# Kernel tuning notes

Measured on AMD Instinct MI355X. Metric: run time of the kernel, lower is better.

## Reference

```python
import jax, jax.numpy as jnp
import numpy as np

NH = 8      # num_head
WIN = 7     # window
EPS = 1e-6


def _ln(x, w, b):
    m = x.mean(-1, keepdims=True)
    v = ((x - m) ** 2).mean(-1, keepdims=True)
    return (x - m) / jnp.sqrt(v + EPS) * w + b


def _dwconv(x, w, b):
    # x: [B,H,W,Cc], w: [7,7,1,Cc] (HWIO), depthwise (groups=Cc)
    y = jax.lax.conv_general_dilated(
        x, w, window_strides=(1, 1), padding='SAME',
        dimension_numbers=('NHWC', 'HWIO', 'NHWC'),
        feature_group_count=x.shape[-1])
    return y + b


def setup_inputs() -> dict:
    B, H, W, C = 16, 56, 56, 256
    RATIO = 8
    key = jax.random.key(0)
    ki = iter(jax.random.split(key, 48))
    def lin(i, o):
        return jax.random.normal(next(ki), (i, o), jnp.float32) * (1.0 / i) ** 0.5
    def bias(o):
        return jnp.zeros((o,), jnp.float32)
    def dw(c):
        return jax.random.normal(next(ki), (7, 7, 1, c), jnp.float32) * 0.05
    inp = {
        'x':   jax.random.normal(next(ki), (B, H, W, C), jnp.float32),
        'x_e': jax.random.normal(next(ki), (B, H, W, C // 2), jnp.float32),
        # LayerNorms
        'norm_w': jnp.ones((C,), jnp.float32),  'norm_b': bias(C),
        'norme_w': jnp.ones((C // 2,), jnp.float32), 'norme_b': bias(C // 2),
        # local_rr path
        'rr1_w': lin(C, C), 'rr1_b': bias(C),
        'rr2_w': lin(C, C), 'rr2_b': bias(C),
        'rr3_w': lin(C, C), 'rr3_b': bias(C),
        'conv_w': dw(C), 'conv_b': bias(C),
        # LocalAttentionRGBT
        'lx_l1_w': lin(C, C // 2), 'lx_l1_b': bias(C // 2),
        'lx_l2_w': lin(C // 2, C // 2), 'lx_l2_b': bias(C // 2),
        'lx_c1_w': dw(C // 2), 'lx_c1_b': bias(C // 2),
        'lx_c2_w': dw(C // 2), 'lx_c2_b': bias(C // 2),
        'lx_fc1_w': lin(C, C // RATIO),  # no bias
        'lx_fc2_w': lin(C // RATIO, C),  # no bias
        'lx_l3_w': lin(C, C // 2), 'lx_l3_b': bias(C // 2),
        # global pooled attention
        'kv_w': lin(C, C), 'kv_b': bias(C),
        'q_w': lin(C // 2 * 3, C // 2), 'q_b': bias(C // 2),
        # output projections (window != 0 => in = 2C)
        'proj_w': lin(2 * C, C), 'proj_b': bias(C),
        'proje_w': lin(2 * C, C // 2), 'proje_b': bias(C // 2),
    }
    return inp


def reference(x, x_e, norm_w, norm_b, norme_w, norme_b,
              rr1_w, rr1_b, rr2_w, rr2_b, rr3_w, rr3_b, conv_w, conv_b,
              lx_l1_w, lx_l1_b, lx_l2_w, lx_l2_b, lx_c1_w, lx_c1_b,
              lx_c2_w, lx_c2_b, lx_fc1_w, lx_fc2_w, lx_l3_w, lx_l3_b,
              kv_w, kv_b, q_w, q_b, proj_w, proj_b, proje_w, proje_b):
    B, H, W, C = x.shape
    hd = C // NH // 2  # head dim
    x = _ln(x, norm_w, norm_b)
    x_e = _ln(x_e, norme_w, norme_b)

    # --- local_rr: gated depthwise-conv branch ---
    rr1 = x @ rr1_w + rr1_b
    rr2 = _dwconv(x @ rr2_w + rr2_b, conv_w, conv_b)
    rr2 = rr2 @ rr3_w + rr3_b
    local_rr = rr1 * rr2  # [B,H,W,C]

    # --- LocalAttentionRGBT: cross-modal cosine-sim channel gate ---
    rgb = x @ lx_l1_w + lx_l1_b      # [B,H,W,C/2]
    t = x_e @ lx_l2_w + lx_l2_b      # [B,H,W,C/2]
    co = _dwconv(rgb * t, lx_c1_w, lx_c1_b)
    di = _dwconv(jnp.abs(rgb - t), lx_c2_w, lx_c2_b)
    co_di = jnp.concatenate([co, di], axis=-1)           # [B,H,W,C]
    amap = co_di.mean(-1, keepdims=True)                 # [B,H,W,1]
    dot = (amap * co_di).sum((1, 2), keepdims=True)      # [B,1,1,C]
    n1 = jnp.sqrt((amap ** 2).sum((1, 2), keepdims=True))
    n2 = jnp.sqrt((co_di ** 2).sum((1, 2), keepdims=True))
    cos_sim = dot / (n1 * n2 + 1e-6)                     # [B,1,1,C]
    attn_c = jax.nn.sigmoid(
        jax.nn.gelu(cos_sim @ lx_fc1_w, approximate=False) @ lx_fc2_w)
    local_rx = (co_di * attn_c) @ lx_l3_w + lx_l3_b      # [B,H,W,C/2]

    # --- global: pooled-q full-kv attention ---
    kv = (x @ kv_w + kv_b).reshape(B, H * W, 2, NH, hd).transpose(2, 0, 3, 1, 4)
    k, v = kv[0], kv[1]                                  # [B,NH,HW,hd]
    rx = jnp.concatenate([x, x_e], axis=-1)              # [B,H,W,3C/2]
    rx_pool = rx.reshape(B, WIN, H // WIN, WIN, W // WIN, -1).mean((2, 4))  # [B,7,7,3C/2]
    q = (rx_pool @ q_w + q_b).reshape(B, WIN * WIN, NH, hd).transpose(0, 2, 1, 3)
    scores = jnp.einsum('bnqd,bnkd->bnqk', q * hd ** -0.5, k)  # [B,NH,49,HW]
    attn = jax.nn.softmax(scores, axis=-1)
    g = jnp.einsum('bnqk,bnkd->bnqd', attn, v)           # [B,NH,49,hd]
    g = g.reshape(B, NH, WIN, WIN, hd).transpose(0, 1, 4, 2, 3).reshape(B, C // 2, WIN, WIN)
    g = jax.image.resize(g, (B, C // 2, H, W), method='bilinear')  # align_corners=False
    g = g.transpose(0, 2, 3, 1)                          # [B,H,W,C/2]

    cat = jnp.concatenate([local_rr, local_rx, g], axis=-1)  # [B,H,W,2C]
    x_e_out = cat @ proje_w + proje_b
    x_out = cat @ proj_w + proj_b
    return (x_out, x_e_out)
```

## Files before the change

### kernel.cpp

```cpp
#include <hip/hip_runtime.h>
#include <hip/hip_bf16.h>
#include <cstdint>
#include <cstddef>

#define N_TOK 50176
#define HWSZ  3136
#define BATCH 16

#define GF_MUL     1
#define GF_ASCALE  2
#define GF_KVSPLIT 4
#define GF_DUAL    8

typedef __hip_bfloat16 bf16;
typedef __attribute__((ext_vector_type(8))) short bf16x8;
typedef __attribute__((ext_vector_type(4))) float f32x4;
typedef __attribute__((ext_vector_type(4))) unsigned short u16x4;

__device__ __forceinline__ void  stf(float* p, size_t i, float v) { p[i] = v; }
__device__ __forceinline__ void  stf(bf16* p, size_t i, float v) { p[i] = __float2bfloat16(v); }
__device__ __forceinline__ float bu2f(unsigned short u) {
    unsigned int x = ((unsigned int)u) << 16; float f; __builtin_memcpy(&f, &x, 4); return f;
}
__device__ __forceinline__ unsigned short f2bu(float f) {
    bf16 t = __float2bfloat16(f); unsigned short u; __builtin_memcpy(&u, &t, 2); return u;
}

struct WtrDesc { const float* src; bf16* dst; int K; int N; int off; };
struct WtrPack { WtrDesc d[9]; int total; };
__global__ __launch_bounds__(256) void wtr_all(WtrPack p)
{
    int idx = blockIdx.x * 256 + threadIdx.x;
    if (idx >= p.total) return;
    #pragma unroll
    for (int s = 0; s < 9; s++) {
        int lo = p.d[s].off, hi = lo + p.d[s].K * p.d[s].N;
        if (idx >= lo && idx < hi) {
            int j = idx - lo;
            int k = j / p.d[s].N, n = j % p.d[s].N;
            p.d[s].dst[(size_t)n * p.d[s].K + k] = __float2bfloat16(p.d[s].src[j]);
        }
    }
}

__global__ __launch_bounds__(256) void ln_kernel(const float* __restrict__ in,
    const float* __restrict__ w, const float* __restrict__ b,
    bf16* __restrict__ out, int rows, int Cdim)
{
    int wave = threadIdx.x >> 6, lane = threadIdx.x & 63;
    int row = blockIdx.x * 4 + wave;
    if (row >= rows) return;
    const float* p = in + (size_t)row * Cdim;
    int nj = Cdim >> 6;
    float v[4];
    float s = 0.f;
    for (int j = 0; j < nj; j++) { v[j] = p[lane + 64 * j]; s += v[j]; }
    for (int off = 32; off; off >>= 1) s += __shfl_xor(s, off, 64);
    float mean = s / (float)Cdim;
    float vs = 0.f;
    for (int j = 0; j < nj; j++) { float d = v[j] - mean; vs += d * d; }
    for (int off = 32; off; off >>= 1) vs += __shfl_xor(vs, off, 64);
    float rstd = 1.f / sqrtf(vs / (float)Cdim + 1e-6f);
    bf16* q = out + (size_t)row * Cdim;
    for (int j = 0; j < nj; j++) {
        int c = lane + 64 * j;
        q[c] = __float2bfloat16((v[j] - mean) * rstd * w[c] + b[c]);
    }
}

#define LDT 56
template<int FLAGS, typename OT>
__global__ __launch_bounds__(256) void gemm_mfma(
    const bf16* __restrict__ A, int lda,
    const bf16* __restrict__ WT,
    const float* __restrict__ bias,
    OT* __restrict__ C, int ldc,
    int M, int K, int N,
    const bf16* __restrict__ mul, int mulld,
    const float* __restrict__ ascale,
    bf16* __restrict__ kout, bf16* __restrict__ vout,
    OT* __restrict__ C2, int ldc2, const float* __restrict__ bias2, int N1)
{
    __shared__ bf16 As[64][LDT];
    __shared__ bf16 Bs[128][LDT];
    int ntile = N >> 7;
    int bid = blockIdx.x;
    bid = (bid & 7) * (gridDim.x >> 3) + (bid >> 3);
    int m0 = (bid / ntile) * 64;
    int n0 = (bid % ntile) * 128;
    int tid = threadIdx.x;
    int lane = tid & 63, wid = tid >> 6;
    int wc = wid * 32;
    int lrow = lane & 15, lko = (lane >> 4) * 8;
    int sr = tid >> 2, sko = (tid & 3) * 8;

    f32x4 acc[4][2];
    #pragma unroll
    for (int i = 0; i < 4; i++)
        #pragma unroll
        for (int j = 0; j < 2; j++)
            acc[i][j] = (f32x4){0.f, 0.f, 0.f, 0.f};

    bf16x8 ra, rb[2];
    {
        bf16x8 v = *reinterpret_cast<const bf16x8*>(A + (size_t)(m0 + sr) * lda + sko);
        if (FLAGS & GF_ASCALE) {
            int bidx = (m0 + sr) / HWSZ;
            const float* as = ascale + (size_t)bidx * K + sko;
            #pragma unroll
            for (int e = 0; e < 8; e++)
                v[e] = (short)f2bu(bu2f((unsigned short)v[e]) * as[e]);
        }
        ra = v;
        rb[0] = *reinterpret_cast<const bf16x8*>(WT + (size_t)(n0 + sr) * K + sko);
        rb[1] = *reinterpret_cast<const bf16x8*>(WT + (size_t)(n0 + sr + 64) * K + sko);
    }

    for (int k0 = 0; k0 < K; k0 += 32) {
        *reinterpret_cast<bf16x8*>(&As[sr][sko]) = ra;
        *reinterpret_cast<bf16x8*>(&Bs[sr][sko]) = rb[0];
        *reinterpret_cast<bf16x8*>(&Bs[sr + 64][sko]) = rb[1];
        __syncthreads();
        int kn = k0 + 32;
        if (kn < K) {
            bf16x8 v = *reinterpret_cast<const bf16x8*>(A + (size_t)(m0 + sr) * lda + kn + sko);
            if (FLAGS & GF_ASCALE) {
                int bidx = (m0 + sr) / HWSZ;
                const float* as = ascale + (size_t)bidx * K + kn + sko;
                #pragma unroll
                for (int e = 0; e < 8; e++)
                    v[e] = (short)f2bu(bu2f((unsigned short)v[e]) * as[e]);
            }
            ra = v;
            rb[0] = *reinterpret_cast<const bf16x8*>(WT + (size_t)(n0 + sr) * K + kn + sko);
            rb[1] = *reinterpret_cast<const bf16x8*>(WT + (size_t)(n0 + sr + 64) * K + kn + sko);
        }
        bf16x8 af[4], br[2];
        #pragma unroll
        for (int i = 0; i < 4; i++)
            af[i] = *reinterpret_cast<const bf16x8*>(&As[i * 16 + lrow][lko]);
        #pragma unroll
        for (int j = 0; j < 2; j++)
            br[j] = *reinterpret_cast<const bf16x8*>(&Bs[wc + j * 16 + lrow][lko]);
        #pragma unroll
        for (int i = 0; i < 4; i++)
            #pragma unroll
            for (int j = 0; j < 2; j++)
                acc[i][j] = __builtin_amdgcn_mfma_f32_16x16x32_bf16(af[i], br[j], acc[i][j], 0, 0, 0);
        __syncthreads();
    }

    int orow = (lane >> 4) * 4;
    int ocol = lane & 15;
    #pragma unroll
    for (int i = 0; i < 4; i++) {
        #pragma unroll
        for (int j = 0; j < 2; j++) {
            #pragma unroll
            for (int p = 0; p < 4; p++) {
                int gm = m0 + i * 16 + orow + p;
                int gn = n0 + wc + j * 16 + ocol;
                if (FLAGS & GF_KVSPLIT) {
                    float v = acc[i][j][p] + bias[gn];
                    int bb = gm / HWSZ, n = gm % HWSZ;
                    if (gn < 128)
                        kout[(((size_t)bb * 8 + (gn >> 4)) * HWSZ + n) * 16 + (gn & 15)] = __float2bfloat16(v);
                    else {
                        int hh = (gn - 128) >> 4, dd = (gn - 128) & 15;
                        vout[(((size_t)bb * 8 + hh) * 16 + dd) * HWSZ + n] = __float2bfloat16(v);
                    }
                } else if (FLAGS & GF_DUAL) {
                    if (gn < N1) {
                        float v = acc[i][j][p] + bias[gn];
                        stf(C, (size_t)gm * ldc + gn, v);
                    } else {
                        float v = acc[i][j][p] + bias2[gn - N1];
                        stf(C2, (size_t)gm * ldc2 + (gn - N1), v);
                    }
                } else {
                    float v = acc[i][j][p] + bias[gn];
                    if (FLAGS & GF_MUL) v *= __bfloat162float(mul[(size_t)gm * mulld + gn]);
                    stf(C, (size_t)gm * ldc + gn, v);
                }
            }
        }
    }
}

__global__ __launch_bounds__(256) void gemm_k(
    const float* __restrict__ A, int lda,
    const float* __restrict__ Wt, const float* __restrict__ bias,
    float* __restrict__ Cc, int ldc, int M, int K, int Nc)
{
    __shared__ float As[16][68];
    __shared__ float Ws[16][64];
    int ntile = Nc >> 6;
    int tile_n = blockIdx.x % ntile;
    int tile_m = blockIdx.x / ntile;
    int m0 = tile_m * 64, n0 = tile_n * 64;
    int tid = threadIdx.x;
    int tx = tid & 15, ty = tid >> 4;
    float acc[4][4] = {};
    for (int k0 = 0; k0 < K; k0 += 16) {
        int ks = tid & 15, ms = tid >> 4;
        #pragma unroll
        for (int i = 0; i < 4; i++) {
            int gm = m0 + ms + i * 16;
            As[ks][ms + i * 16] = (gm < M) ? A[(size_t)gm * lda + k0 + ks] : 0.f;
        }
        #pragma unroll
        for (int j = 0; j < 4; j++) {
            int k = (tid >> 6) * 4 + j;
            Ws[k][tid & 63] = Wt[(size_t)(k0 + k) * Nc + n0 + (tid & 63)];
        }
        __syncthreads();
        #pragma unroll
        for (int k = 0; k < 16; k++) {
            float a[4], w[4];
            #pragma unroll
            for (int i = 0; i < 4; i++) a[i] = As[k][ty * 4 + i];
            #pragma unroll
            for (int j = 0; j < 4; j++) w[j] = Ws[k][tx * 4 + j];
            #pragma unroll
            for (int i = 0; i < 4; i++)
                #pragma unroll
                for (int j = 0; j < 4; j++)
                    acc[i][j] += a[i] * w[j];
        }
        __syncthreads();
    }
    #pragma unroll
    for (int i = 0; i < 4; i++) {
        int gm = m0 + ty * 4 + i;
        if (gm >= M) continue;
        #pragma unroll
        for (int j = 0; j < 4; j++) {
            int gn = n0 + tx * 4 + j;
            Cc[(size_t)gm * ldc + gn] = acc[i][j] + bias[gn];
        }
    }
}

__global__ __launch_bounds__(256) void dwconv_reg(const bf16* __restrict__ in,
    bf16* __restrict__ out,
    const float* __restrict__ w0, const float* __restrict__ b0,
    const float* __restrict__ w1, const float* __restrict__ b1, int split)
{
    int tid = threadIdx.x;
    int chg = tid & 31;
    int bsw = (blockIdx.x & 7) * 196 + (blockIdx.x >> 3);
    int pg  = bsw * 8 + (tid >> 5);
    int xg = pg % 14;
    int y  = (pg / 14) % 56;
    int b  = pg / (14 * 56);
    int c0 = chg * 8;
    int x0 = xg * 4;

    const float* wp; const float* bp; int ws, cw;
    if (c0 < split) { wp = w0; bp = b0; ws = split;       cw = c0; }
    else            { wp = w1; bp = b1; ws = 256 - split; cw = c0 - split; }

    float acc[4][8];
    #pragma unroll
    for (int o = 0; o < 4; o++)
        #pragma unroll
        for (int e = 0; e < 8; e++) acc[o][e] = 0.f;

    const bf16* base = in + (size_t)b * HWSZ * 256 + c0;
    const float* wbase = wp + cw;
    #pragma unroll
    for (int ky = 0; ky < 7; ky++) {
        int gy = y + ky - 3;
        if (gy < 0 || gy >= 56) continue;
        const bf16* rowp = base + (size_t)gy * 56 * 256;
        float cf[10][8];
        #pragma unroll
        for (int j = 0; j < 10; j++) {
            int gx = x0 + j - 3;
            bf16x8 v = {0, 0, 0, 0, 0, 0, 0, 0};
            if ((unsigned)gx < 56u)
                v = *reinterpret_cast<const bf16x8*>(rowp + (size_t)gx * 256);
            #pragma unroll
            for (int e = 0; e < 8; e++) cf[j][e] = bu2f((unsigned short)v[e]);
        }
        const float* wrow = wbase + ky * 7 * ws;
        #pragma unroll
        for (int kx = 0; kx < 7; kx++) {
            float4 wa = *reinterpret_cast<const float4*>(wrow + kx * ws);
            float4 wb = *reinterpret_cast<const float4*>(wrow + kx * ws + 4);
            #pragma unroll
            for (int o = 0; o < 4; o++) {
                acc[o][0] += cf[o + kx][0] * wa.x;
                acc[o][1] += cf[o + kx][1] * wa.y;
                acc[o][2] += cf[o + kx][2] * wa.z;
                acc[o][3] += cf[o + kx][3] * wa.w;
                acc[o][4] += cf[o + kx][4] * wb.x;
                acc[o][5] += cf[o + kx][5] * wb.y;
                acc[o][6] += cf[o + kx][6] * wb.z;
                acc[o][7] += cf[o + kx][7] * wb.w;
            }
        }
    }

    float4 ba = *reinterpret_cast<const float4*>(bp + cw);
    float4 bb = *reinterpret_cast<const float4*>(bp + cw + 4);
    bf16* obase = out + (((size_t)b * HWSZ + (size_t)y * 56 + x0) * 256) + c0;
    #pragma unroll
    for (int o = 0; o < 4; o++) {
        bf16x8 ov;
        ov[0] = (short)f2bu(acc[o][0] + ba.x);
        ov[1] = (short)f2bu(acc[o][1] + ba.y);
        ov[2] = (short)f2bu(acc[o][2] + ba.z);
        ov[3] = (short)f2bu(acc[o][3] + ba.w);
        ov[4] = (short)f2bu(acc[o][4] + bb.x);
        ov[5] = (short)f2bu(acc[o][5] + bb.y);
        ov[6] = (short)f2bu(acc[o][6] + bb.z);
        ov[7] = (short)f2bu(acc[o][7] + bb.w);
        *reinterpret_cast<bf16x8*>(obase + (size_t)o * 256) = ov;
    }
}

__global__ void rgbt_k(const bf16* __restrict__ rgb, const bf16* __restrict__ t,
                       bf16* __restrict__ codin, int total )
{
    int i = blockIdx.x * blockDim.x + threadIdx.x;
    if (i >= total) return;
    int n = i >> 7, c = i & 127;
    float a = __bfloat162float(rgb[i]), bb = __bfloat162float(t[i]);
    codin[(size_t)n * 256 + c] = __float2bfloat16(a * bb);
    codin[(size_t)n * 256 + 128 + c] = __float2bfloat16(fabsf(a - bb));
}

__global__ __launch_bounds__(256) void cosred_k(const bf16* __restrict__ codi,
    float* __restrict__ part)
{
    int b = blockIdx.x >> 4;
    int bi = blockIdx.x & 15;
    int wave = threadIdx.x >> 6, lane = threadIdx.x & 63;
    int slot = bi * 4 + wave;
    float dloc[4] = {0,0,0,0}, n2loc[4] = {0,0,0,0};
    float n1loc = 0.f;
    for (int i = 0; i < 49; i++) {
        int p = slot * 49 + i;
        const bf16* row = codi + ((size_t)b * HWSZ + p) * 256;
        float v[4]; float sum = 0.f;
        #pragma unroll
        for (int j = 0; j < 4; j++) { v[j] = __bfloat162float(row[lane + 64 * j]); sum += v[j]; }
        for (int off = 32; off; off >>= 1) sum += __shfl_xor(sum, off, 64);
        float amap = sum * (1.f / 256.f);
        #pragma unroll
        for (int j = 0; j < 4; j++) { dloc[j] += amap * v[j]; n2loc[j] += v[j] * v[j]; }
        n1loc += amap * amap;
    }
    float* dst = part + ((size_t)b * 64 + slot) * 513;
    #pragma unroll
    for (int j = 0; j < 4; j++) {
        dst[lane + 64 * j] = dloc[j];
        dst[256 + lane + 64 * j] = n2loc[j];
    }
    if (lane == 0) dst[512] = n1loc;
}

__global__ __launch_bounds__(256) void mlp_kernel(const float* __restrict__ part,
    const float* __restrict__ fc1w, const float* __restrict__ fc2w,
    float* __restrict__ attnc)
{
    int b = blockIdx.x;
    int tid = threadIdx.x;
    __shared__ float cosb[256];
    __shared__ float hbuf[32];
    const float* pb = part + (size_t)b * 64 * 513;
    float dot = 0.f, n2 = 0.f, n1 = 0.f;
    for (int s = 0; s < 64; s++) {
        dot += pb[s * 513 + tid];
        n2  += pb[s * 513 + 256 + tid];
        n1  += pb[s * 513 + 512];
    }
    float cs = dot / (sqrtf(n1) * sqrtf(n2) + 1e-6f);
    cosb[tid] = cs;
    __syncthreads();
    if (tid < 32) {
        float h = 0.f;
        for (int c = 0; c < 256; c++) h += cosb[c] * fc1w[c * 32 + tid];
        h = 0.5f * h * (1.f + erff(h * 0.70710678f));
        hbuf[tid] = h;
    }
    __syncthreads();
    float o = 0.f;
    for (int j = 0; j < 32; j++) o += hbuf[j] * fc2w[j * 256 + tid];
    attnc[b * 256 + tid] = 1.f / (1.f + expf(-o));
}

__global__ __launch_bounds__(384) void pool_kernel(const bf16* __restrict__ xn,
    const bf16* __restrict__ xen, float* __restrict__ rxpool)
{
    int bij = blockIdx.x;
    int b = bij / 49; int ij = bij % 49; int i = ij / 7, j = ij % 7;
    int c = threadIdx.x;
    float s = 0.f;
    for (int dy = 0; dy < 8; dy++)
        for (int dx = 0; dx < 8; dx++) {
            size_t n = ((size_t)b * 56 + (i * 8 + dy)) * 56 + (j * 8 + dx);
            s += (c < 256) ? __bfloat162float(xn[n * 256 + c])
                           : __bfloat162float(xen[n * 128 + (c - 256)]);
        }
    rxpool[(size_t)bij * 384 + c] = s * (1.f / 64.f);
}

#define NSPLIT 14
#define POSB   224
__global__ __launch_bounds__(256) void attn_mfma(const float* __restrict__ qbuf,
    const bf16* __restrict__ kbuf, const bf16* __restrict__ vtbuf,
    float* __restrict__ osplit, float* __restrict__ mlbuf)
{
    int bh = blockIdx.x & 127;
    int split = blockIdx.x >> 7;
    int b = bh >> 3, h = bh & 7;
    int tid = threadIdx.x;
    int qt = tid >> 6;
    int lane = tid & 63;
    int lo = lane & 15, hi = lane >> 4;

    bf16x8 qf = {0, 0, 0, 0, 0, 0, 0, 0};
    int q = qt * 16 + lo;
    if (hi < 2 && q < 49) {
        const float* qp = qbuf + ((size_t)b * 49 + q) * 128 + h * 16 + hi * 8;
        #pragma unroll
        for (int j = 0; j < 8; j++) qf[j] = (short)f2bu(qp[j] * 0.25f);
    }
    const bf16* kbase = kbuf + (size_t)bh * HWSZ * 16;
    const bf16* vbase = vtbuf + ((size_t)bh * 16 + lo) * HWSZ;

    float m_run = -1e30f, l_run = 0.f;
    f32x4 oacc = {0.f, 0.f, 0.f, 0.f};
    int pos1 = 8 * (lo >> 2) + (lo & 3);
    const f32x4 zz = {0.f, 0.f, 0.f, 0.f};

    for (int t = 0; t < POSB / 32; t++) {
        int base = split * POSB + t * 32;
        bf16x8 kf1 = {0, 0, 0, 0, 0, 0, 0, 0}, kf2 = kf1;
        if (hi < 2) {
            kf1 = *reinterpret_cast<const bf16x8*>(kbase + (size_t)(base + pos1) * 16 + hi * 8);
            kf2 = *reinterpret_cast<const bf16x8*>(kbase + (size_t)(base + pos1 + 4) * 16 + hi * 8);
        }
        bf16x8 vf = *reinterpret_cast<const bf16x8*>(vbase + base + hi * 8);
        f32x4 s1 = __builtin_amdgcn_mfma_f32_16x16x32_bf16(kf1, qf, zz, 0, 0, 0);
        f32x4 s2 = __builtin_amdgcn_mfma_f32_16x16x32_bf16(kf2, qf, zz, 0, 0, 0);
        float pmax = fmaxf(fmaxf(fmaxf(s1[0], s1[1]), fmaxf(s1[2], s1[3])),
                           fmaxf(fmaxf(s2[0], s2[1]), fmaxf(s2[2], s2[3])));
        pmax = fmaxf(pmax, __shfl_xor(pmax, 16, 64));
        pmax = fmaxf(pmax, __shfl_xor(pmax, 32, 64));
        float mnew = fmaxf(m_run, pmax);
        float esc = __expf(m_run - mnew);
        l_run *= esc;
        float e0 = __shfl(esc, 4 * hi + 0, 64);
        float e1 = __shfl(esc, 4 * hi + 1, 64);
        float e2 = __shfl(esc, 4 * hi + 2, 64);
        float e3 = __shfl(esc, 4 * hi + 3, 64);
        oacc[0] *= e0; oacc[1] *= e1; oacc[2] *= e2; oacc[3] *= e3;
        float p0 = __expf(s1[0] - mnew), p1 = __expf(s1[1] - mnew);
        float p2 = __expf(s1[2] - mnew), p3 = __expf(s1[3] - mnew);
        float p4 = __expf(s2[0] - mnew), p5 = __expf(s2[1] - mnew);
        float p6 = __expf(s2[2] - mnew), p7 = __expf(s2[3] - mnew);
        float rs = ((p0 + p1) + (p2 + p3)) + ((p4 + p5) + (p6 + p7));
        rs += __shfl_xor(rs, 16, 64);
        rs += __shfl_xor(rs, 32, 64);
        l_run += rs;
        m_run = mnew;
        bf16x8 pf;
        pf[0] = (short)f2bu(p0); pf[1] = (short)f2bu(p1);
        pf[2] = (short)f2bu(p2); pf[3] = (short)f2bu(p3);
        pf[4] = (short)f2bu(p4); pf[5] = (short)f2bu(p5);
        pf[6] = (short)f2bu(p6); pf[7] = (short)f2bu(p7);
        oacc = __builtin_amdgcn_mfma_f32_16x16x32_bf16(pf, vf, oacc, 0, 0, 0);
    }

    float* ob = osplit + ((size_t)bh * NSPLIT + split) * 64 * 16;
    #pragma unroll
    for (int r = 0; r < 4; r++) {
        int qq = qt * 16 + 4 * hi + r;
        ob[(size_t)qq * 16 + lo] = oacc[r];
    }
    if (hi == 0) {
        float* mlb = mlbuf + (((size_t)bh * NSPLIT + split) * 64 + qt * 16 + lo) * 2;
        mlb[0] = m_run; mlb[1] = l_run;
    }
}

__global__ __launch_bounds__(256) void attn_combine(const float* __restrict__ osplit,
    const float* __restrict__ mlbuf, float* __restrict__ gs)
{
    int idx = blockIdx.x * 256 + threadIdx.x;
    if (idx >= 128 * 49 * 16) return;
    int d = idx & 15;
    int pq = idx >> 4;
    int bh = pq / 49, q = pq % 49;
    float m[NSPLIT], l[NSPLIT];
    float M = -1e30f;
    #pragma unroll
    for (int s = 0; s < NSPLIT; s++) {
        const float* mlb = mlbuf + (((size_t)bh * NSPLIT + s) * 64 + q) * 2;
        m[s] = mlb[0]; l[s] = mlb[1];
        M = fmaxf(M, m[s]);
    }
    float L = 0.f, O = 0.f;
    #pragma unroll
    for (int s = 0; s < NSPLIT; s++) {
        float e = __expf(m[s] - M);
        L += l[s] * e;
        O += osplit[(((size_t)bh * NSPLIT + s) * 64 + q) * 16 + d] * e;
    }
    gs[(size_t)pq * 16 + d] = O / L;
}

__global__ void upsample_kernel(const float* __restrict__ gs, bf16* __restrict__ cat)
{
    int idx = blockIdx.x * blockDim.x + threadIdx.x;
    if (idx >= N_TOK * 128) return;
    int c = idx & 127;
    int pos = idx >> 7;
    int h = c >> 4, d = c & 15;
    int x = pos % 56;
    int y = (pos / 56) % 56;
    int b = pos / HWSZ;
    float sy = (y + 0.5f) * 0.125f - 0.5f;
    float sx = (x + 0.5f) * 0.125f - 0.5f;
    int y0f = (int)floorf(sy); float wy = sy - (float)y0f;
    int x0f = (int)floorf(sx); float wx = sx - (float)x0f;
    int y0 = max(0, min(6, y0f)), y1 = max(0, min(6, y0f + 1));
    int x0 = max(0, min(6, x0f)), x1 = max(0, min(6, x0f + 1));
    const float* g0 = gs + ((size_t)(b * 8 + h) * 49) * 16 + d;
    float v00 = g0[(y0 * 7 + x0) * 16], v01 = g0[(y0 * 7 + x1) * 16];
    float v10 = g0[(y1 * 7 + x0) * 16], v11 = g0[(y1 * 7 + x1) * 16];
    float v0 = v00 + (v01 - v00) * wx;
    float v1 = v10 + (v11 - v10) * wx;
    float v = v0 + (v1 - v0) * wy;
    cat[(size_t)pos * 512 + 384 + c] = __float2bfloat16(v);
}

extern "C" void kernel_launch(void* const* d_in, const int* in_sizes, int n_in,
                              void* d_out, int out_size, void* d_ws, size_t ws_size,
                              hipStream_t stream)
{
    const float* x      = (const float*)d_in[0];
    const float* x_e    = (const float*)d_in[1];
    const float* norm_w = (const float*)d_in[2];
    const float* norm_b = (const float*)d_in[3];
    const float* norme_w= (const float*)d_in[4];
    const float* norme_b= (const float*)d_in[5];
    const float* rr1_w  = (const float*)d_in[6];
    const float* rr1_b  = (const float*)d_in[7];
    const float* rr2_w  = (const float*)d_in[8];
    const float* rr2_b  = (const float*)d_in[9];
    const float* rr3_w  = (const float*)d_in[10];
    const float* rr3_b  = (const float*)d_in[11];
    const float* conv_w = (const float*)d_in[12];
    const float* conv_b = (const float*)d_in[13];
    const float* l1_w   = (const float*)d_in[14];
    const float* l1_b   = (const float*)d_in[15];
    const float* l2_w   = (const float*)d_in[16];
    const float* l2_b   = (const float*)d_in[17];
    const float* c1_w   = (const float*)d_in[18];
    const float* c1_b   = (const float*)d_in[19];
    const float* c2_w   = (const float*)d_in[20];
    const float* c2_b   = (const float*)d_in[21];
    const float* fc1_w  = (const float*)d_in[22];
    const float* fc2_w  = (const float*)d_in[23];
    const float* l3_w   = (const float*)d_in[24];
    const float* l3_b   = (const float*)d_in[25];
    const float* kv_w   = (const float*)d_in[26];
    const float* kv_b   = (const float*)d_in[27];
    const float* q_w    = (const float*)d_in[28];
    const float* q_b    = (const float*)d_in[29];
    const float* proj_w = (const float*)d_in[30];
    const float* proj_b = (const float*)d_in[31];
    const float* proje_w= (const float*)d_in[32];
    const float* proje_b= (const float*)d_in[33];

    float* part   = (float*)d_ws;
    float* attnc  = part   + (size_t)525312;
    float* gs     = attnc  + 4096;
    float* rxpool = gs     + 100352;
    float* qbuf   = rxpool + 301056;
    bf16* wt      = (bf16*)(qbuf + 100352);
    bf16* rr1_t  = wt;
    bf16* rr2_t  = rr1_t + 65536;
    bf16* rr3_t  = rr2_t + 65536;
    bf16* kv_t   = rr3_t + 65536;
    bf16* l1_t   = kv_t  + 65536;
    bf16* l2_t   = l1_t  + 32768;
    bf16* l3_t   = l2_t  + 16384;
    bf16* proj_t = l3_t  + 32768;
    bf16* proje_t= proj_t + 131072;
    bf16* xn     = proje_t + 65536;
    bf16* xen    = xn   + (size_t)N_TOK * 256;
    bf16* bufC   = xen  + (size_t)N_TOK * 128;
    bf16* bufD   = bufC + (size_t)N_TOK * 256;
    bf16* bufE   = bufD + (size_t)N_TOK * 256;
    bf16* cat    = bufE + (size_t)N_TOK * 256;
    size_t need = (size_t)((char*)(cat + (size_t)N_TOK * 512) - (char*)d_ws);
    if (ws_size < need) return;

    bf16* kbuf = bufC;
    bf16* vbuf = bufC + (size_t)N_TOK * 128;

    float* osplit = (float*)bufD;
    float* mlbuf  = osplit + (size_t)128 * NSPLIT * 64 * 16;

    float* xout  = (float*)d_out;
    float* xeout = xout + (size_t)N_TOK * 256;

    const int nthr = 256;
    auto mgrid = [](int M, int N) { return dim3((M / 64) * (N / 128)); };

    {
        WtrPack p;
        const float* srcs[9] = {rr1_w, rr2_w, rr3_w, kv_w, l1_w, l2_w, l3_w, proj_w, proje_w};
        bf16* dsts[9] = {rr1_t, rr2_t, rr3_t, kv_t, l1_t, l2_t, l3_t, proj_t, proje_t};
        int Ks[9] = {256, 256, 256, 256, 256, 128, 256, 512, 512};
        int Ns[9] = {256, 256, 256, 256, 128, 128, 128, 256, 128};
        int off = 0;
        for (int s = 0; s < 9; s++) {
            p.d[s] = {srcs[s], dsts[s], Ks[s], Ns[s], off};
            off += Ks[s] * Ns[s];
        }
        p.total = off;
        wtr_all<<<dim3((off + 255) / 256), dim3(256), 0, stream>>>(p);
    }

    ln_kernel<<<dim3(N_TOK / 4), dim3(nthr), 0, stream>>>(x, norm_w, norm_b, xn, N_TOK, 256);
    ln_kernel<<<dim3(N_TOK / 4), dim3(nthr), 0, stream>>>(x_e, norme_w, norme_b, xen, N_TOK, 128);

    gemm_mfma<GF_DUAL, bf16><<<mgrid(N_TOK, 512), dim3(nthr), 0, stream>>>(
        xn, 256, rr1_t, rr1_b, bufC, 256, N_TOK, 256, 512, nullptr, 0, nullptr, nullptr, nullptr,
        bufD, 256, rr2_b, 256);
    dwconv_reg<<<dim3(N_TOK / 32), dim3(nthr), 0, stream>>>(
        bufD, bufE, conv_w, conv_b, conv_w, conv_b, 256);
    gemm_mfma<GF_MUL, bf16><<<mgrid(N_TOK, 256), dim3(nthr), 0, stream>>>(
        bufE, 256, rr3_t, rr3_b, cat, 512, N_TOK, 256, 256, bufC, 256, nullptr, nullptr, nullptr,
        nullptr, 0, nullptr, 0);

    gemm_mfma<0, bf16><<<mgrid(N_TOK, 128), dim3(nthr), 0, stream>>>(
        xn, 256, l1_t, l1_b, bufD, 128, N_TOK, 256, 128, nullptr, 0, nullptr, nullptr, nullptr,
        nullptr, 0, nullptr, 0);
    gemm_mfma<0, bf16><<<mgrid(N_TOK, 128), dim3(nthr), 0, stream>>>(
        xen, 128, l2_t, l2_b, bufD + (size_t)N_TOK * 128, 128, N_TOK, 128, 128, nullptr, 0, nullptr, nullptr, nullptr,
        nullptr, 0, nullptr, 0);
    rgbt_k<<<dim3((N_TOK * 128) / nthr), dim3(nthr), 0, stream>>>(
        bufD, bufD + (size_t)N_TOK * 128, bufC, N_TOK * 128);
    dwconv_reg<<<dim3(N_TOK / 32), dim3(nthr), 0, stream>>>(
        bufC, bufE, c1_w, c1_b, c2_w, c2_b, 128);
    cosred_k<<<dim3(BATCH * 16), dim3(nthr), 0, stream>>>(bufE, part);
    mlp_kernel<<<dim3(BATCH), dim3(nthr), 0, stream>>>(part, fc1_w, fc2_w, attnc);
    gemm_mfma<GF_ASCALE, bf16><<<mgrid(N_TOK, 128), dim3(nthr), 0, stream>>>(
        bufE, 256, l3_t, l3_b, cat + 256, 512, N_TOK, 256, 128, nullptr, 0, attnc, nullptr, nullptr,
        nullptr, 0, nullptr, 0);

    gemm_mfma<GF_KVSPLIT, bf16><<<mgrid(N_TOK, 256), dim3(nthr), 0, stream>>>(
        xn, 256, kv_t, kv_b, (bf16*)nullptr, 0, N_TOK, 256, 256, nullptr, 0, nullptr, kbuf, vbuf,
        nullptr, 0, nullptr, 0);
    pool_kernel<<<dim3(BATCH * 49), dim3(384), 0, stream>>>(xn, xen, rxpool);
    gemm_k<<<dim3(((784 + 63) / 64) * 2), dim3(nthr), 0, stream>>>(
        rxpool, 384, q_w, q_b, qbuf, 128, 784, 384, 128);
    attn_mfma<<<dim3(128 * NSPLIT), dim3(nthr), 0, stream>>>(qbuf, kbuf, vbuf, osplit, mlbuf);
    attn_combine<<<dim3(392), dim3(nthr), 0, stream>>>(osplit, mlbuf, gs);
    upsample_kernel<<<dim3((N_TOK * 128) / nthr), dim3(nthr), 0, stream>>>(gs, cat);

    gemm_mfma<GF_DUAL, float><<<mgrid(N_TOK, 384), dim3(nthr), 0, stream>>>(
        cat, 512, proj_t, proj_b, xout, 256, N_TOK, 512, 384, nullptr, 0, nullptr, nullptr, nullptr,
        xeout, 128, proje_b, 256);
}
```

Baseline: 433.9 us.

## Double-buffer GEMM shared-memory tiles with two-stage register prefetch

Splits the MFMA GEMM's LDS tiles into two ping-pong buffers and keeps two register prefetch stages in flight. This cuts the barriers per K-step from two to one and lets global loads run further ahead of compute. The LDS row pitch also shrinks from 56 to 40 elements to hold the doubled footprint, which changes the bank-conflict pattern. The loop assumes K is a multiple of 64 and adds register pressure.

New measurement: 428.1 us. Within noise of the previous version (-1.3%).

```diff
diff --git a/kernel.cpp b/kernel.cpp
--- a/kernel.cpp
+++ b/kernel.cpp
@@ -68,7 +68,7 @@
     }
 }
 
-#define LDT 56
+#define LDT 40
 template<int FLAGS, typename OT>
 __global__ __launch_bounds__(256) void gemm_mfma(
     const bf16* __restrict__ A, int lda,
@@ -81,8 +81,8 @@
     bf16* __restrict__ kout, bf16* __restrict__ vout,
     OT* __restrict__ C2, int ldc2, const float* __restrict__ bias2, int N1)
 {
-    __shared__ bf16 As[64][LDT];
-    __shared__ bf16 Bs[128][LDT];
+    __shared__ bf16 As[2][64][LDT];
+    __shared__ bf16 Bs[2][128][LDT];
     int ntile = N >> 7;
     int bid = blockIdx.x;
     bid = (bid & 7) * (gridDim.x >> 3) + (bid >> 3);
@@ -101,54 +101,53 @@
         for (int j = 0; j < 2; j++)
             acc[i][j] = (f32x4){0.f, 0.f, 0.f, 0.f};
 
-    bf16x8 ra, rb[2];
-    {
-        bf16x8 v = *reinterpret_cast<const bf16x8*>(A + (size_t)(m0 + sr) * lda + sko);
-        if (FLAGS & GF_ASCALE) {
-            int bidx = (m0 + sr) / HWSZ;
-            const float* as = ascale + (size_t)bidx * K + sko;
-            #pragma unroll
-            for (int e = 0; e < 8; e++)
-                v[e] = (short)f2bu(bu2f((unsigned short)v[e]) * as[e]);
-        }
-        ra = v;
-        rb[0] = *reinterpret_cast<const bf16x8*>(WT + (size_t)(n0 + sr) * K + sko);
-        rb[1] = *reinterpret_cast<const bf16x8*>(WT + (size_t)(n0 + sr + 64) * K + sko);
-    }
-
-    for (int k0 = 0; k0 < K; k0 += 32) {
-        *reinterpret_cast<bf16x8*>(&As[sr][sko]) = ra;
-        *reinterpret_cast<bf16x8*>(&Bs[sr][sko]) = rb[0];
-        *reinterpret_cast<bf16x8*>(&Bs[sr + 64][sko]) = rb[1];
+#define GLOAD(RA, RB0, RB1, KOFF) do {                                                        \
+    bf16x8 v_ = *reinterpret_cast<const bf16x8*>(A + (size_t)(m0 + sr) * lda + (KOFF) + sko); \
+    if (FLAGS & GF_ASCALE) {                                                                  \
+        int bidx_ = (m0 + sr) / HWSZ;                                                         \
+        const float* as_ = ascale + (size_t)bidx_ * K + (KOFF) + sko;                         \
+        for (int e_ = 0; e_ < 8; e_++)                                                        \
+            v_[e_] = (short)f2bu(bu2f((unsigned short)v_[e_]) * as_[e_]);                     \
+    }                                                                                         \
+    RA = v_;                                                                                  \
+    RB0 = *reinterpret_cast<const bf16x8*>(WT + (size_t)(n0 + sr) * K + (KOFF) + sko);        \
+    RB1 = *reinterpret_cast<const bf16x8*>(WT + (size_t)(n0 + sr + 64) * K + (KOFF) + sko);   \
+} while (0)
+
+#define GWRITE(P, RA, RB0, RB1) do {                                   \
+    *reinterpret_cast<bf16x8*>(&As[P][sr][sko]) = RA;                  \
+    *reinterpret_cast<bf16x8*>(&Bs[P][sr][sko]) = RB0;                 \
+    *reinterpret_cast<bf16x8*>(&Bs[P][sr + 64][sko]) = RB1;            \
+} while (0)
+
+#define GCOMP(P) do {                                                                         \
+    bf16x8 af_[4], br_[2];                                                                    \
+    for (int i_ = 0; i_ < 4; i_++)                                                            \
+        af_[i_] = *reinterpret_cast<const bf16x8*>(&As[P][i_ * 16 + lrow][lko]);              \
+    for (int j_ = 0; j_ < 2; j_++)                                                            \
+        br_[j_] = *reinterpret_cast<const bf16x8*>(&Bs[P][wc + j_ * 16 + lrow][lko]);         \
+    for (int i_ = 0; i_ < 4; i_++)                                                            \
+        for (int j_ = 0; j_ < 2; j_++)                                                        \
+            acc[i_][j_] = __builtin_amdgcn_mfma_f32_16x16x32_bf16(af_[i_], br_[j_], acc[i_][j_], 0, 0, 0); \
+} while (0)
+
+    bf16x8 ra0, rb00, rb01, ra1, rb10, rb11;
+    GLOAD(ra0, rb00, rb01, 0);
+    GLOAD(ra1, rb10, rb11, 32);
+    int nst = K >> 5;
+    for (int s = 0; s < nst; s += 2) {
+        GWRITE(0, ra0, rb00, rb01);
+        if (s + 2 < nst) GLOAD(ra0, rb00, rb01, (s + 2) * 32);
         __syncthreads();
-        int kn = k0 + 32;
-        if (kn < K) {
-            bf16x8 v = *reinterpret_cast<const bf16x8*>(A + (size_t)(m0 + sr) * lda + kn + sko);
-            if (FLAGS & GF_ASCALE) {
-                int bidx = (m0 + sr) / HWSZ;
-                const float* as = ascale + (size_t)bidx * K + kn + sko;
-                #pragma unroll
-                for (int e = 0; e < 8; e++)
-                    v[e] = (short)f2bu(bu2f((unsigned short)v[e]) * as[e]);
-            }
-            ra = v;
-            rb[0] = *reinterpret_cast<const bf16x8*>(WT + (size_t)(n0 + sr) * K + kn + sko);
-            rb[1] = *reinterpret_cast<const bf16x8*>(WT + (size_t)(n0 + sr + 64) * K + kn + sko);
-        }
-        bf16x8 af[4], br[2];
-        #pragma unroll
-        for (int i = 0; i < 4; i++)
-            af[i] = *reinterpret_cast<const bf16x8*>(&As[i * 16 + lrow][lko]);
-        #pragma unroll
-        for (int j = 0; j < 2; j++)
-            br[j] = *reinterpret_cast<const bf16x8*>(&Bs[wc + j * 16 + lrow][lko]);
-        #pragma unroll
-        for (int i = 0; i < 4; i++)
-            #pragma unroll
-            for (int j = 0; j < 2; j++)
-                acc[i][j] = __builtin_amdgcn_mfma_f32_16x16x32_bf16(af[i], br[j], acc[i][j], 0, 0, 0);
+        GCOMP(0);
+        GWRITE(1, ra1, rb10, rb11);
+        if (s + 3 < nst) GLOAD(ra1, rb10, rb11, (s + 3) * 32);
         __syncthreads();
-    }
+        GCOMP(1);
+    }
+#undef GLOAD
+#undef GWRITE
+#undef GCOMP
 
     int orow = (lane >> 4) * 4;
     int ocol = lane & 15;
```
